# Optimization experiments

Measured on AMD Instinct MI355X. Metric: run time of the kernel, lower is better.

The kernel has to match this reference:

```python
import jax, jax.numpy as jnp
import numpy as np

HIDDEN = 2048
N_HEADS = 16
N_KV_HEADS = 4
HEAD_DIM = 128
N_REP = N_HEADS // N_KV_HEADS
BATCH = 2
SEQ = 2048
SCALE = HEAD_DIM ** -0.5
NEG = -1e9


def apply_rope(x, freqs):
    # x: (b, s, h, d); freqs: (s, d//2) angles. Interleaved-pair rotation.
    cos = jnp.cos(freqs)[None, :, None, :]
    sin = jnp.sin(freqs)[None, :, None, :]
    x1 = x[..., 0::2]
    x2 = x[..., 1::2]
    r1 = x1 * cos - x2 * sin
    r2 = x1 * sin + x2 * cos
    return jnp.stack([r1, r2], axis=-1).reshape(x.shape)


def setup_inputs() -> dict:
    key = jax.random.key(0)
    ks = jax.random.split(key, 6)
    x = jax.random.normal(ks[0], (BATCH, SEQ, HIDDEN), dtype=jnp.float32)
    wq = jax.random.normal(ks[1], (N_HEADS * HEAD_DIM, HIDDEN), dtype=jnp.float32) * 0.02
    wk = jax.random.normal(ks[2], (N_KV_HEADS * HEAD_DIM, HIDDEN), dtype=jnp.float32) * 0.02
    wv = jax.random.normal(ks[3], (N_KV_HEADS * HEAD_DIM, HIDDEN), dtype=jnp.float32) * 0.02
    wo = jax.random.normal(ks[4], (HIDDEN, N_HEADS * HEAD_DIM), dtype=jnp.float32) * 0.02
    # RoPE angle table: pos * theta^{-2i/d}
    inv_freq = 1.0 / (10000.0 ** (jnp.arange(0, HEAD_DIM, 2, dtype=jnp.float32) / HEAD_DIM))
    rope_freqs = jnp.arange(SEQ, dtype=jnp.float32)[:, None] * inv_freq[None, :]  # (S, d/2)
    # additive causal mask
    causal = jnp.tril(jnp.ones((SEQ, SEQ), dtype=bool))
    mask = jnp.where(causal, 0.0, NEG).astype(jnp.float32)[None, None]  # (1,1,S,S)
    return {"x": x, "wq": wq, "wk": wk, "wv": wv, "wo": wo,
            "rope_freqs": rope_freqs, "mask": mask}


def reference(x, wq, wk, wv, wo, rope_freqs, mask):
    b, s, _ = x.shape
    q = (x @ wq.T).reshape(b, s, N_HEADS, HEAD_DIM)
    k = (x @ wk.T).reshape(b, s, N_KV_HEADS, HEAD_DIM)
    v = (x @ wv.T).reshape(b, s, N_KV_HEADS, HEAD_DIM)
    q = apply_rope(q, rope_freqs)
    k = apply_rope(k, rope_freqs)
    new_k, new_v = k, v  # kv cache (no prior cache, start_pos=0)
    # GQA: repeat each kv head n_rep times (matches expand+reshape in source)
    k_rep = jnp.repeat(k, N_REP, axis=2)  # (b, s, n_heads, d)
    v_rep = jnp.repeat(v, N_REP, axis=2)
    scores = jnp.einsum('bqhd,bkhd->bhqk', q, k_rep) * SCALE
    scores = scores + mask
    attn = jax.nn.softmax(scores.astype(jnp.float32), axis=-1).astype(q.dtype)
    out = jnp.einsum('bhqk,bkhd->bqhd', attn, v_rep).reshape(b, s, -1)
    return out @ wo.T, (new_k, new_v)
```

## Files before the change

### kernel.cpp

```cpp
#include <hip/hip_runtime.h>
#include <hip/hip_bf16.h>

#define NH 16
#define NKV 4
#define HD 128
#define QSCALE 0.1275174272f

using bf16x8 = __attribute__((ext_vector_type(8))) __bf16;
using f32x4  = __attribute__((ext_vector_type(4))) float;
using u16x8  = __attribute__((ext_vector_type(8))) unsigned short;
using u16x2  = __attribute__((ext_vector_type(2))) unsigned short;

__device__ __forceinline__ unsigned short f2b(float f) {
  __hip_bfloat16 h = __float2bfloat16(f);
  return __builtin_bit_cast(unsigned short, h);
}
__device__ __forceinline__ float b2f(unsigned short u) {
  unsigned int v = ((unsigned int)u) << 16;
  return __builtin_bit_cast(float, v);
}

__device__ __forceinline__ void glds16(const unsigned short* g, unsigned short* l) {
  __builtin_amdgcn_global_load_lds(
      (const __attribute__((address_space(1))) unsigned int*)(const void*)g,
      (__attribute__((address_space(3))) unsigned int*)(void*)l, 16, 0, 0);
}

__global__ __launch_bounds__(256) void cvt_fused(const float* __restrict__ x,
                                                 const float* __restrict__ wq,
                                                 const float* __restrict__ wk,
                                                 const float* __restrict__ wv,
                                                 const float* __restrict__ wo,
                                                 unsigned short* __restrict__ xb,
                                                 unsigned short* __restrict__ wqkvb,
                                                 unsigned short* __restrict__ wob) {
  int i = blockIdx.x * 256 + threadIdx.x;
  const float* src;
  unsigned short* dst;
  int off;
  if (i < 1048576)      { src = x;  dst = xb;              off = i; }
  else if (i < 1572864) { src = wq; dst = wqkvb;           off = i - 1048576; }
  else if (i < 1703936) { src = wk; dst = wqkvb + 4194304; off = i - 1572864; }
  else if (i < 1835008) { src = wv; dst = wqkvb + 5242880; off = i - 1703936; }
  else                  { src = wo; dst = wob;             off = i - 1835008; }
  const float4* s4 = reinterpret_cast<const float4*>(src) + (size_t)off * 2;
  float4 v0 = s4[0], v1 = s4[1];
  u16x8 o;
  o[0] = f2b(v0.x); o[1] = f2b(v0.y); o[2] = f2b(v0.z); o[3] = f2b(v0.w);
  o[4] = f2b(v1.x); o[5] = f2b(v1.y); o[6] = f2b(v1.z); o[7] = f2b(v1.w);
  reinterpret_cast<u16x8*>(dst)[off] = o;
}

template<int CF32, int BN>
__global__ __launch_bounds__(512, 1) void gemm_full(const unsigned short* __restrict__ A,
                                                    const unsigned short* __restrict__ B,
                                                    void* __restrict__ C,
                                                    int N, int K, int nbx) {
  constexpr int BM = 128;
  constexpr int AF = 4;
  constexpr int BF = BN / 64;
  constexpr int BH = BF / 2;
  constexpr int AL = 1;
  constexpr int BL = BN / 128;
  __shared__ unsigned short As[3][BM * 32];
  __shared__ unsigned short Bs[3][BN * 32];
  const int tid = threadIdx.x, lane = tid & 63;
  const int wid = tid >> 6, wm = wid >> 2, wn = wid & 3;
  const int cpx = gridDim.x >> 3;
  const int wgid = (blockIdx.x & 7) * cpx + (blockIdx.x >> 3);
  const int bx = wgid % nbx, by = wgid / nbx;
  const int row0 = by * BM, col0 = bx * BN;
  const int fr = lane & 15, g = lane >> 4;
  const int NT = K >> 5;

  size_t offA;
  {
    int cid = tid, R = cid >> 3, phys = cid & 7, cl = phys ^ (R & 7);
    offA = (size_t)(row0 + 2 * R + (cl >> 2)) * K + (cl & 3) * 8;
  }
  size_t offB[BL];
#pragma unroll
  for (int l = 0; l < BL; l++) {
    int cid = tid + l * 512, R = cid >> 3, phys = cid & 7, cl = phys ^ (R & 7);
    offB[l] = (size_t)(col0 + 2 * R + (cl >> 2)) * K + (cl & 3) * 8;
  }

  auto stage_p0 = [&](int t, int sb) {
    int k0 = t * 32;
    glds16(A + offA + k0, &As[sb][tid * 8]);
    glds16(B + offB[0] + k0, &Bs[sb][tid * 8]);
  };
  auto stage_p1 = [&](int t, int sb) {
    int k0 = t * 32;
#pragma unroll
    for (int l = 1; l < BL; l++)
      glds16(B + offB[l] + k0, &Bs[sb][(tid + l * 512) * 8]);
  };

  auto ldfrag = [&](const unsigned short* buf, int row) {
    int R = row >> 1;
    int phys = ((((row & 1) << 2) | g) ^ (R & 7));
    return *reinterpret_cast<const bf16x8*>(&buf[R * 64 + phys * 8]);
  };

  f32x4 acc[AF][BF];
#pragma unroll
  for (int i = 0; i < AF; i++)
#pragma unroll
    for (int j = 0; j < BF; j++) acc[i][j] = f32x4{0.f, 0.f, 0.f, 0.f};

  stage_p0(0, 0); stage_p1(0, 0);
  stage_p0(1, 1); stage_p1(1, 1);
  if constexpr (AL + BL == 4) asm volatile("s_waitcnt vmcnt(4)" ::: "memory");
  else                        asm volatile("s_waitcnt vmcnt(3)" ::: "memory");
  __builtin_amdgcn_s_barrier();
  __builtin_amdgcn_sched_barrier(0);

  int rb = 0, sb = 2;
#pragma unroll 1
  for (int t = 0; t < NT; ++t) {
    const unsigned short* Ar = &As[rb][0];
    const unsigned short* Br = &Bs[rb][0];

    bf16x8 af[AF], bfr[BF];
#pragma unroll
    for (int mf = 0; mf < AF; mf++) af[mf] = ldfrag(Ar, wm * 64 + mf * 16 + fr);
#pragma unroll
    for (int nf = 0; nf < BH; nf++) bfr[nf] = ldfrag(Br, wn * (BN / 4) + nf * 16 + fr);
    if (t + 2 < NT) stage_p0(t + 2, sb);
    __builtin_amdgcn_s_barrier();
    asm volatile("s_waitcnt lgkmcnt(0)" ::: "memory");
    __builtin_amdgcn_sched_barrier(0);
    __builtin_amdgcn_s_setprio(1);
#pragma unroll
    for (int mf = 0; mf < AF; mf++)
#pragma unroll
      for (int nf = 0; nf < BH; nf++)
        acc[mf][nf] = __builtin_amdgcn_mfma_f32_16x16x32_bf16(af[mf], bfr[nf], acc[mf][nf], 0, 0, 0);
    __builtin_amdgcn_s_setprio(0);
    __builtin_amdgcn_sched_barrier(0);
    __builtin_amdgcn_s_barrier();

#pragma unroll
    for (int nf = BH; nf < BF; nf++) bfr[nf] = ldfrag(Br, wn * (BN / 4) + nf * 16 + fr);
    if (t + 2 < NT) stage_p1(t + 2, sb);
    __builtin_amdgcn_s_barrier();
    asm volatile("s_waitcnt lgkmcnt(0)" ::: "memory");
    __builtin_amdgcn_sched_barrier(0);
    __builtin_amdgcn_s_setprio(1);
#pragma unroll
    for (int mf = 0; mf < AF; mf++)
#pragma unroll
      for (int nf = BH; nf < BF; nf++)
        acc[mf][nf] = __builtin_amdgcn_mfma_f32_16x16x32_bf16(af[mf], bfr[nf], acc[mf][nf], 0, 0, 0);
    __builtin_amdgcn_s_setprio(0);
    __builtin_amdgcn_sched_barrier(0);

    if (t + 1 < NT) {
      if (t + 2 < NT) {
        if constexpr (AL + BL == 4) asm volatile("s_waitcnt vmcnt(4)" ::: "memory");
        else                        asm volatile("s_waitcnt vmcnt(3)" ::: "memory");
      } else {
        asm volatile("s_waitcnt vmcnt(0)" ::: "memory");
      }
      __builtin_amdgcn_s_barrier();
      __builtin_amdgcn_sched_barrier(0);
    }
    rb = rb == 2 ? 0 : rb + 1;
    sb = sb == 2 ? 0 : sb + 1;
  }

#pragma unroll
  for (int i = 0; i < AF; i++) {
#pragma unroll
    for (int j = 0; j < BF; j++) {
      int rbase = row0 + wm * 64 + i * 16 + g * 4;
      int cb = col0 + wn * (BN / 4) + j * 16 + fr;
#pragma unroll
      for (int r = 0; r < 4; r++) {
        if (CF32)
          reinterpret_cast<float*>(C)[(size_t)(rbase + r) * N + cb] = acc[i][j][r];
        else
          reinterpret_cast<unsigned short*>(C)[(size_t)(rbase + r) * N + cb] = f2b(acc[i][j][r]);
      }
    }
  }
}

__global__ __launch_bounds__(256) void rope_kernel(const unsigned short* __restrict__ qkv,
                                                   const float* __restrict__ freqs,
                                                   unsigned short* __restrict__ qro,
                                                   unsigned short* __restrict__ kro,
                                                   float* __restrict__ newk) {
  const int NQ = 4096 * 16 * 64;
  const int NK = 4096 * 4 * 64;
  int idx = blockIdx.x * 256 + threadIdx.x;
  if (idx >= NQ + NK) return;
  if (idx < NQ) {
    int i = idx & 63;
    int h = (idx >> 6) & 15;
    int row = idx >> 10;
    int s = row & 2047, b = row >> 11;
    float f = freqs[s * 64 + i];
    float c = cosf(f), sn = sinf(f);
    u16x2 xv = *reinterpret_cast<const u16x2*>(qkv + (size_t)row * 3072 + h * 128 + 2 * i);
    float x1 = b2f(xv.x), x2 = b2f(xv.y);
    float r1 = (x1 * c - x2 * sn) * QSCALE;
    float r2 = (x1 * sn + x2 * c) * QSCALE;
    u16x2 o; o.x = f2b(r1); o.y = f2b(r2);
    *reinterpret_cast<u16x2*>(qro + ((size_t)(b * 16 + h) * 2048 + s) * 128 + 2 * i) = o;
  } else {
    idx -= NQ;
    int i = idx & 63;
    int h = (idx >> 6) & 3;
    int row = idx >> 8;
    int s = row & 2047, b = row >> 11;
    float f = freqs[s * 64 + i];
    float c = cosf(f), sn = sinf(f);
    u16x2 xv = *reinterpret_cast<const u16x2*>(qkv + (size_t)row * 3072 + 2048 + h * 128 + 2 * i);
    float x1 = b2f(xv.x), x2 = b2f(xv.y);
    float r1 = x1 * c - x2 * sn;
    float r2 = x1 * sn + x2 * c;
    u16x2 o; o.x = f2b(r1); o.y = f2b(r2);
    *reinterpret_cast<u16x2*>(kro + ((size_t)(b * 4 + h) * 2048 + s) * 128 + 2 * i) = o;
    float2 of; of.x = r1; of.y = r2;
    *reinterpret_cast<float2*>(newk + (size_t)row * 512 + h * 128 + 2 * i) = of;
  }
}

__global__ __launch_bounds__(256) void vtrans_kernel(const unsigned short* __restrict__ qkv,
                                                     unsigned short* __restrict__ vt,
                                                     float* __restrict__ newv) {
  __shared__ unsigned short T[32][136];
  const int st = blockIdx.x;
  const int kvh = blockIdx.y & 3, b = blockIdx.y >> 2;
  const int s0 = st * 32;
  const int t = threadIdx.x;
  const int ls = t >> 3;
  const int ch = (t & 7) * 2;
  const unsigned short* src = qkv + (size_t)(b * 2048 + s0 + ls) * 3072 + 2560 + kvh * 128 + ch * 8;
  u16x8 a0 = *reinterpret_cast<const u16x8*>(src);
  u16x8 a1 = *reinterpret_cast<const u16x8*>(src + 8);
  *reinterpret_cast<u16x8*>(&T[ls][ch * 8])     = a0;
  *reinterpret_cast<u16x8*>(&T[ls][ch * 8 + 8]) = a1;
  float* nv = newv + (size_t)(b * 2048 + s0 + ls) * 512 + kvh * 128 + ch * 8;
  float4 f0, f1, f2, f3;
  f0.x = b2f(a0[0]); f0.y = b2f(a0[1]); f0.z = b2f(a0[2]); f0.w = b2f(a0[3]);
  f1.x = b2f(a0[4]); f1.y = b2f(a0[5]); f1.z = b2f(a0[6]); f1.w = b2f(a0[7]);
  f2.x = b2f(a1[0]); f2.y = b2f(a1[1]); f2.z = b2f(a1[2]); f2.w = b2f(a1[3]);
  f3.x = b2f(a1[4]); f3.y = b2f(a1[5]); f3.z = b2f(a1[6]); f3.w = b2f(a1[7]);
  reinterpret_cast<float4*>(nv)[0] = f0;
  reinterpret_cast<float4*>(nv)[1] = f1;
  reinterpret_cast<float4*>(nv)[2] = f2;
  reinterpret_cast<float4*>(nv)[3] = f3;
  __syncthreads();
  const int d = t >> 1, half = t & 1;
  unsigned short* dst = vt + ((size_t)(b * 4 + kvh) * 128 + d) * 2048 + s0 + half * 16;
  u16x8 o0, o1;
#pragma unroll
  for (int q = 0; q < 8; q++) {
    int slot = half * 16 + q;
    int kl = ((slot >> 2) & 1) * 16 + (slot >> 3) * 4 + (slot & 3);
    o0[q] = T[kl][d];
  }
#pragma unroll
  for (int q = 0; q < 8; q++) {
    int slot = half * 16 + 8 + q;
    int kl = ((slot >> 2) & 1) * 16 + (slot >> 3) * 4 + (slot & 3);
    o1[q] = T[kl][d];
  }
  reinterpret_cast<u16x8*>(dst)[0] = o0;
  reinterpret_cast<u16x8*>(dst)[1] = o1;
}

__global__ __launch_bounds__(256, 4) void attn_kernel(const unsigned short* __restrict__ qro,
                                                      const unsigned short* __restrict__ kro,
                                                      const unsigned short* __restrict__ vt,
                                                      unsigned short* __restrict__ out) {
  __shared__ unsigned short Ks[2][32 * 128];
  __shared__ unsigned short Vs[2][64 * 64];
  const int tid = threadIdx.x, lane = tid & 63, w = tid >> 6;
  const int kvhb = blockIdx.x & 7;
  const int kvh = kvhb & 3, b = kvhb >> 2;
  const int t = 127 - (blockIdx.x >> 3);
  const int h = kvh * 4 + w;
  const int qbase = t * 16;
  const int fr = lane & 15, g = lane >> 4, fk = g * 8;
  const unsigned short* Kp = kro + (size_t)(b * 4 + kvh) * 2048 * 128;
  const unsigned short* Vtp = vt + (size_t)(b * 4 + kvh) * 128 * 2048;
  const unsigned short* Qp = qro + ((size_t)(b * 16 + h) * 2048 + qbase) * 128;

  bf16x8 qf[4];
#pragma unroll
  for (int kk = 0; kk < 4; kk++)
    qf[kk] = *reinterpret_cast<const bf16x8*>(Qp + fr * 128 + kk * 32 + fk);

  u16x8 onesu;
#pragma unroll
  for (int j = 0; j < 8; j++) onesu[j] = 0x3F80;
  bf16x8 ones = __builtin_bit_cast(bf16x8, onesu);

  f32x4 o[8];
#pragma unroll
  for (int dt = 0; dt < 8; dt++) o[dt] = f32x4{0.f, 0.f, 0.f, 0.f};
  f32x4 dacc = f32x4{0.f, 0.f, 0.f, 0.f};
  const int qrow_s = qbase + fr;
  const int nfull = (qbase >= 31) ? ((qbase - 31) >> 5) + 1 : 0;
  const int niter = nfull + 1;

  const int krow = w * 8 + (lane >> 4);
  const int kcol = lane & 15;
  const int vrow = w * 16 + (lane >> 3);
  const int vcol = lane & 7;

  auto stage = [&](int kv0, int buf) {
    unsigned short* Kb = &Ks[buf][0];
    unsigned short* Vb = &Vs[buf][0];
#pragma unroll
    for (int j = 0; j < 2; j++) {
      int r = krow + j * 4;
      glds16(Kp + (size_t)(kv0 + r) * 128 + ((kcol ^ (r & 7)) * 8),
             Kb + (w * 8 + j * 4) * 128);
    }
#pragma unroll
    for (int j = 0; j < 2; j++) {
      int r = vrow + j * 8;
      int u = vcol ^ (r & 7);
      int d = 2 * r + (u >> 2);
      glds16(Vtp + (size_t)d * 2048 + kv0 + (u & 3) * 8,
             Vb + (w * 16 + j * 8) * 64);
    }
  };

  auto step = [&](int kv0, bool mask, int buf) {
    const unsigned short* Kb = &Ks[buf][0];
    const unsigned short* Vb = &Vs[buf][0];
    f32x4 sc[2];
    sc[0] = sc[1] = f32x4{0.f, 0.f, 0.f, 0.f};
    __builtin_amdgcn_s_setprio(1);
#pragma unroll
    for (int kk = 0; kk < 4; kk++) {
      int blk = ((kk * 4 + g) ^ (fr & 7)) * 8;
      bf16x8 ka0 = *reinterpret_cast<const bf16x8*>(Kb + (fr +  0) * 128 + blk);
      bf16x8 ka1 = *reinterpret_cast<const bf16x8*>(Kb + (fr + 16) * 128 + blk);
      sc[0] = __builtin_amdgcn_mfma_f32_16x16x32_bf16(ka0, qf[kk], sc[0], 0, 0, 0);
      sc[1] = __builtin_amdgcn_mfma_f32_16x16x32_bf16(ka1, qf[kk], sc[1], 0, 0, 0);
    }
    __builtin_amdgcn_s_setprio(0);
#pragma unroll
    for (int s = 0; s < 2; s++)
#pragma unroll
      for (int r = 0; r < 4; r++) {
        float v = sc[s][r];
        if (mask && (kv0 + 16 * s + 4 * g + r > qrow_s)) v = -1e30f;
        sc[s][r] = __builtin_amdgcn_exp2f(v);
      }
    u16x8 pau;
#pragma unroll
    for (int j = 0; j < 4; j++) {
      pau[j]     = f2b(sc[0][j]);
      pau[4 + j] = f2b(sc[1][j]);
    }
    bf16x8 pa = __builtin_bit_cast(bf16x8, pau);
    dacc = __builtin_amdgcn_mfma_f32_16x16x32_bf16(pa, ones, dacc, 0, 0, 0);
    __builtin_amdgcn_s_setprio(1);
#pragma unroll
    for (int dt = 0; dt < 8; dt++) {
      int jr = dt * 8 + (fr >> 1);
      int c = ((fr & 1) * 4 + g) ^ (fr >> 1);
      bf16x8 vf = *reinterpret_cast<const bf16x8*>(Vb + jr * 64 + c * 8);
      o[dt] = __builtin_amdgcn_mfma_f32_16x16x32_bf16(pa, vf, o[dt], 0, 0, 0);
    }
    __builtin_amdgcn_s_setprio(0);
  };

  stage(0, 0);
  int buf = 0;
  for (int i = 0; i < niter; i++) {
    __syncthreads();
    if (i + 1 < niter) stage((i + 1) * 32, buf ^ 1);
    step(i * 32, i == nfull, buf);
    buf ^= 1;
  }

#pragma unroll
  for (int r = 0; r < 4; r++) {
    float inv = 1.0f / dacc[r];
    int qrow = qbase + g * 4 + r;
    size_t rowoff = ((size_t)b * 2048 + qrow) * 2048 + (size_t)h * 128;
#pragma unroll
    for (int dt = 0; dt < 8; dt++)
      out[rowoff + dt * 16 + fr] = f2b(o[dt][r] * inv);
  }
}

extern "C" void kernel_launch(void* const* d_in, const int* in_sizes, int n_in,
                              void* d_out, int out_size, void* d_ws, size_t ws_size,
                              hipStream_t stream) {
  const float* x  = (const float*)d_in[0];
  const float* wq = (const float*)d_in[1];
  const float* wk = (const float*)d_in[2];
  const float* wv = (const float*)d_in[3];
  const float* wo = (const float*)d_in[4];
  const float* freqs = (const float*)d_in[5];

  char* ws = (char*)d_ws;
  unsigned short* xb    = (unsigned short*)(ws);
  unsigned short* attn  = xb;
  unsigned short* wqkvb = (unsigned short*)(ws + 16777216);
  unsigned short* wob   = (unsigned short*)(ws + 29360128);
  unsigned short* qkv   = (unsigned short*)(ws + 37748736);
  unsigned short* qro   = (unsigned short*)(ws + 62914560);
  unsigned short* kro   = (unsigned short*)(ws + 79691776);
  unsigned short* vt    = (unsigned short*)(ws + 83886080);

  float* out_o = (float*)d_out;
  float* out_k = (float*)d_out + 8388608;
  float* out_v = (float*)d_out + 10485760;

  cvt_fused<<<9216, 256, 0, stream>>>(x, wq, wk, wv, wo, xb, wqkvb, wob);

  gemm_full<0, 384><<<256, 512, 0, stream>>>(xb, wqkvb, qkv, 3072, 2048, 8);

  rope_kernel<<<20480, 256, 0, stream>>>(qkv, freqs, qro, kro, out_k);
  vtrans_kernel<<<dim3(64, 8), 256, 0, stream>>>(qkv, vt, out_v);

  attn_kernel<<<1024, 256, 0, stream>>>(qro, kro, vt, attn);

  gemm_full<1, 256><<<256, 512, 0, stream>>>(attn, wob, out_o, 2048, 2048, 8);
}
```

Measured before the change: 206.2 us.

## Process 32 query rows per warp in attention to reuse K/V tiles

Each warp now handles two 16-row query sub-tiles instead of one, so every K and V fragment loaded from shared memory feeds twice as many MFMAs. The grid is halved to 512 blocks and launch bounds drop to 2 blocks per SM to make room for the doubled accumulators. This targets LDS/global traffic per FLOP in the attention kernel. In exchange it uses more registers, gives lower occupancy, adds some wasted masked work on the diagonal tile, and leaves fewer blocks to balance the causal workload.

```diff
diff --git a/kernel.cpp b/kernel.cpp
--- a/kernel.cpp
+++ b/kernel.cpp
@@ -273,7 +273,7 @@
   reinterpret_cast<u16x8*>(dst)[1] = o1;
 }
 
-__global__ __launch_bounds__(256, 4) void attn_kernel(const unsigned short* __restrict__ qro,
+__global__ __launch_bounds__(256, 2) void attn_kernel(const unsigned short* __restrict__ qro,
                                                       const unsigned short* __restrict__ kro,
                                                       const unsigned short* __restrict__ vt,
                                                       unsigned short* __restrict__ out) {
@@ -282,31 +282,33 @@
   const int tid = threadIdx.x, lane = tid & 63, w = tid >> 6;
   const int kvhb = blockIdx.x & 7;
   const int kvh = kvhb & 3, b = kvhb >> 2;
-  const int t = 127 - (blockIdx.x >> 3);
+  const int t = 63 - (blockIdx.x >> 3);
   const int h = kvh * 4 + w;
-  const int qbase = t * 16;
+  const int qbase = t * 32;
   const int fr = lane & 15, g = lane >> 4, fk = g * 8;
   const unsigned short* Kp = kro + (size_t)(b * 4 + kvh) * 2048 * 128;
   const unsigned short* Vtp = vt + (size_t)(b * 4 + kvh) * 128 * 2048;
   const unsigned short* Qp = qro + ((size_t)(b * 16 + h) * 2048 + qbase) * 128;
 
-  bf16x8 qf[4];
-#pragma unroll
-  for (int kk = 0; kk < 4; kk++)
-    qf[kk] = *reinterpret_cast<const bf16x8*>(Qp + fr * 128 + kk * 32 + fk);
+  bf16x8 qf0[4], qf1[4];
+#pragma unroll
+  for (int kk = 0; kk < 4; kk++) {
+    qf0[kk] = *reinterpret_cast<const bf16x8*>(Qp + fr * 128 + kk * 32 + fk);
+    qf1[kk] = *reinterpret_cast<const bf16x8*>(Qp + (16 + fr) * 128 + kk * 32 + fk);
+  }
 
   u16x8 onesu;
 #pragma unroll
   for (int j = 0; j < 8; j++) onesu[j] = 0x3F80;
   bf16x8 ones = __builtin_bit_cast(bf16x8, onesu);
 
-  f32x4 o[8];
-#pragma unroll
-  for (int dt = 0; dt < 8; dt++) o[dt] = f32x4{0.f, 0.f, 0.f, 0.f};
-  f32x4 dacc = f32x4{0.f, 0.f, 0.f, 0.f};
-  const int qrow_s = qbase + fr;
-  const int nfull = (qbase >= 31) ? ((qbase - 31) >> 5) + 1 : 0;
-  const int niter = nfull + 1;
+  f32x4 o0[8], o1[8];
+#pragma unroll
+  for (int dt = 0; dt < 8; dt++) { o0[dt] = f32x4{0.f, 0.f, 0.f, 0.f}; o1[dt] = f32x4{0.f, 0.f, 0.f, 0.f}; }
+  f32x4 dacc0 = f32x4{0.f, 0.f, 0.f, 0.f};
+  f32x4 dacc1 = f32x4{0.f, 0.f, 0.f, 0.f};
+  const int qrow0 = qbase + fr, qrow1 = qbase + 16 + fr;
+  const int niter = t + 1;
 
   const int krow = w * 8 + (lane >> 4);
   const int kcol = lane & 15;
@@ -335,41 +337,53 @@
   auto step = [&](int kv0, bool mask, int buf) {
     const unsigned short* Kb = &Ks[buf][0];
     const unsigned short* Vb = &Vs[buf][0];
-    f32x4 sc[2];
-    sc[0] = sc[1] = f32x4{0.f, 0.f, 0.f, 0.f};
+    f32x4 sA[2], sB[2];
+    sA[0] = sA[1] = f32x4{0.f, 0.f, 0.f, 0.f};
+    sB[0] = sB[1] = f32x4{0.f, 0.f, 0.f, 0.f};
     __builtin_amdgcn_s_setprio(1);
 #pragma unroll
     for (int kk = 0; kk < 4; kk++) {
       int blk = ((kk * 4 + g) ^ (fr & 7)) * 8;
       bf16x8 ka0 = *reinterpret_cast<const bf16x8*>(Kb + (fr +  0) * 128 + blk);
       bf16x8 ka1 = *reinterpret_cast<const bf16x8*>(Kb + (fr + 16) * 128 + blk);
-      sc[0] = __builtin_amdgcn_mfma_f32_16x16x32_bf16(ka0, qf[kk], sc[0], 0, 0, 0);
-      sc[1] = __builtin_amdgcn_mfma_f32_16x16x32_bf16(ka1, qf[kk], sc[1], 0, 0, 0);
+      sA[0] = __builtin_amdgcn_mfma_f32_16x16x32_bf16(ka0, qf0[kk], sA[0], 0, 0, 0);
+      sB[0] = __builtin_amdgcn_mfma_f32_16x16x32_bf16(ka0, qf1[kk], sB[0], 0, 0, 0);
+      sA[1] = __builtin_amdgcn_mfma_f32_16x16x32_bf16(ka1, qf0[kk], sA[1], 0, 0, 0);
+      sB[1] = __builtin_amdgcn_mfma_f32_16x16x32_bf16(ka1, qf1[kk], sB[1], 0, 0, 0);
     }
     __builtin_amdgcn_s_setprio(0);
 #pragma unroll
-    for (int s = 0; s < 2; s++)
+    for (int hh = 0; hh < 2; hh++)
 #pragma unroll
       for (int r = 0; r < 4; r++) {
-        float v = sc[s][r];
-        if (mask && (kv0 + 16 * s + 4 * g + r > qrow_s)) v = -1e30f;
-        sc[s][r] = __builtin_amdgcn_exp2f(v);
+        int kvidx = kv0 + 16 * hh + 4 * g + r;
+        float vA = sA[hh][r];
+        float vB = sB[hh][r];
+        if (mask && (kvidx > qrow0)) vA = -1e30f;
+        if (mask && (kvidx > qrow1)) vB = -1e30f;
+        sA[hh][r] = __builtin_amdgcn_exp2f(vA);
+        sB[hh][r] = __builtin_amdgcn_exp2f(vB);
       }
-    u16x8 pau;
+    u16x8 pau, pbu;
 #pragma unroll
     for (int j = 0; j < 4; j++) {
-      pau[j]     = f2b(sc[0][j]);
-      pau[4 + j] = f2b(sc[1][j]);
+      pau[j]     = f2b(sA[0][j]);
+      pau[4 + j] = f2b(sA[1][j]);
+      pbu[j]     = f2b(sB[0][j]);
+      pbu[4 + j] = f2b(sB[1][j]);
     }
     bf16x8 pa = __builtin_bit_cast(bf16x8, pau);
-    dacc = __builtin_amdgcn_mfma_f32_16x16x32_bf16(pa, ones, dacc, 0, 0, 0);
+    bf16x8 pb = __builtin_bit_cast(bf16x8, pbu);
+    dacc0 = __builtin_amdgcn_mfma_f32_16x16x32_bf16(pa, ones, dacc0, 0, 0, 0);
+    dacc1 = __builtin_amdgcn_mfma_f32_16x16x32_bf16(pb, ones, dacc1, 0, 0, 0);
     __builtin_amdgcn_s_setprio(1);
 #pragma unroll
     for (int dt = 0; dt < 8; dt++) {
       int jr = dt * 8 + (fr >> 1);
       int c = ((fr & 1) * 4 + g) ^ (fr >> 1);
       bf16x8 vf = *reinterpret_cast<const bf16x8*>(Vb + jr * 64 + c * 8);
-      o[dt] = __builtin_amdgcn_mfma_f32_16x16x32_bf16(pa, vf, o[dt], 0, 0, 0);
+      o0[dt] = __builtin_amdgcn_mfma_f32_16x16x32_bf16(pa, vf, o0[dt], 0, 0, 0);
+      o1[dt] = __builtin_amdgcn_mfma_f32_16x16x32_bf16(pb, vf, o1[dt], 0, 0, 0);
     }
     __builtin_amdgcn_s_setprio(0);
   };
@@ -379,18 +393,23 @@
   for (int i = 0; i < niter; i++) {
     __syncthreads();
     if (i + 1 < niter) stage((i + 1) * 32, buf ^ 1);
-    step(i * 32, i == nfull, buf);
+    step(i * 32, i == niter - 1, buf);
     buf ^= 1;
   }
 
 #pragma unroll
   for (int r = 0; r < 4; r++) {
-    float inv = 1.0f / dacc[r];
-    int qrow = qbase + g * 4 + r;
-    size_t rowoff = ((size_t)b * 2048 + qrow) * 2048 + (size_t)h * 128;
-#pragma unroll
-    for (int dt = 0; dt < 8; dt++)
-      out[rowoff + dt * 16 + fr] = f2b(o[dt][r] * inv);
+    float inv0 = 1.0f / dacc0[r];
+    float inv1 = 1.0f / dacc1[r];
+    int q0 = qbase + g * 4 + r;
+    int q1 = qbase + 16 + g * 4 + r;
+    size_t ro0 = ((size_t)b * 2048 + q0) * 2048 + (size_t)h * 128;
+    size_t ro1 = ((size_t)b * 2048 + q1) * 2048 + (size_t)h * 128;
+#pragma unroll
+    for (int dt = 0; dt < 8; dt++) {
+      out[ro0 + dt * 16 + fr] = f2b(o0[dt][r] * inv0);
+      out[ro1 + dt * 16 + fr] = f2b(o1[dt][r] * inv1);
+    }
   }
 }
 
@@ -425,7 +444,7 @@
   rope_kernel<<<20480, 256, 0, stream>>>(qkv, freqs, qro, kro, out_k);
   vtrans_kernel<<<dim3(64, 8), 256, 0, stream>>>(qkv, vt, out_v);
 
-  attn_kernel<<<1024, 256, 0, stream>>>(qro, kro, vt, attn);
+  attn_kernel<<<512, 256, 0, stream>>>(qro, kro, vt, attn);
 
   gemm_full<1, 256><<<256, 512, 0, stream>>>(attn, wob, out_o, 2048, 2048, 8);
 }
```

New measurement: 214.1 us. 1.04x slower.

## Fuse RoPE, V transpose and KV cache writes into QKV GEMM epilogue

Applied to the files above, without the earlier changes.

The standalone rope and V-transpose kernels are removed. The QKV GEMM epilogue now applies RoPE using lane shuffles for the interleaved pairs, writes the rotated Q and K plus the fp32 new_k, and stores the transposed bf16 V along with the fp32 new_v. A cos/sin table is precomputed inside the conversion kernel. This removes the bf16 qkv intermediate round-trip and two kernel launches, at the cost of scattered 2-byte epilogue stores and extra table loads in the GEMM.

```diff
diff --git a/kernel.cpp b/kernel.cpp
--- a/kernel.cpp
+++ b/kernel.cpp
@@ -9,6 +9,7 @@
 using bf16x8 = __attribute__((ext_vector_type(8))) __bf16;
 using f32x4  = __attribute__((ext_vector_type(4))) float;
 using u16x8  = __attribute__((ext_vector_type(8))) unsigned short;
+using u16x4  = __attribute__((ext_vector_type(4))) unsigned short;
 using u16x2  = __attribute__((ext_vector_type(2))) unsigned short;
 
 __device__ __forceinline__ unsigned short f2b(float f) {
@@ -31,10 +32,19 @@
                                                  const float* __restrict__ wk,
                                                  const float* __restrict__ wv,
                                                  const float* __restrict__ wo,
+                                                 const float* __restrict__ freqs,
                                                  unsigned short* __restrict__ xb,
                                                  unsigned short* __restrict__ wqkvb,
-                                                 unsigned short* __restrict__ wob) {
+                                                 unsigned short* __restrict__ wob,
+                                                 float2* __restrict__ cs_tab) {
   int i = blockIdx.x * 256 + threadIdx.x;
+  if (i >= 2359296) {
+    int k = i - 2359296;
+    float f = freqs[k];
+    float2 cs; cs.x = cosf(f); cs.y = sinf(f);
+    cs_tab[k] = cs;
+    return;
+  }
   const float* src;
   unsigned short* dst;
   int off;
@@ -49,6 +59,172 @@
   o[0] = f2b(v0.x); o[1] = f2b(v0.y); o[2] = f2b(v0.z); o[3] = f2b(v0.w);
   o[4] = f2b(v1.x); o[5] = f2b(v1.y); o[6] = f2b(v1.z); o[7] = f2b(v1.w);
   reinterpret_cast<u16x8*>(dst)[off] = o;
+}
+
+__global__ __launch_bounds__(512, 1) void gemm_qkv(const unsigned short* __restrict__ A,
+                                                   const unsigned short* __restrict__ B,
+                                                   const float2* __restrict__ cs_tab,
+                                                   unsigned short* __restrict__ qro,
+                                                   unsigned short* __restrict__ kro,
+                                                   unsigned short* __restrict__ vt,
+                                                   float* __restrict__ newk,
+                                                   float* __restrict__ newv,
+                                                   int K) {
+  constexpr int BN = 384;
+  constexpr int AF = 4, BF = 6, BH = 3, BL = 3;
+  __shared__ unsigned short As[3][128 * 32];
+  __shared__ unsigned short Bs[3][BN * 32];
+  const int tid = threadIdx.x, lane = tid & 63;
+  const int wid = tid >> 6, wm = wid >> 2, wn = wid & 3;
+  const int cpx = gridDim.x >> 3;
+  const int wgid = (blockIdx.x & 7) * cpx + (blockIdx.x >> 3);
+  const int bx = wgid % 8, by = wgid / 8;
+  const int row0 = by * 128, col0 = bx * BN;
+  const int fr = lane & 15, g = lane >> 4;
+  const int NT = K >> 5;
+
+  size_t offA;
+  {
+    int cid = tid, R = cid >> 3, phys = cid & 7, cl = phys ^ (R & 7);
+    offA = (size_t)(row0 + 2 * R + (cl >> 2)) * K + (cl & 3) * 8;
+  }
+  size_t offB[BL];
+#pragma unroll
+  for (int l = 0; l < BL; l++) {
+    int cid = tid + l * 512, R = cid >> 3, phys = cid & 7, cl = phys ^ (R & 7);
+    offB[l] = (size_t)(col0 + 2 * R + (cl >> 2)) * K + (cl & 3) * 8;
+  }
+
+  auto stage_p0 = [&](int t, int sb) {
+    int k0 = t * 32;
+    glds16(A + offA + k0, &As[sb][tid * 8]);
+    glds16(B + offB[0] + k0, &Bs[sb][tid * 8]);
+  };
+  auto stage_p1 = [&](int t, int sb) {
+    int k0 = t * 32;
+#pragma unroll
+    for (int l = 1; l < BL; l++)
+      glds16(B + offB[l] + k0, &Bs[sb][(tid + l * 512) * 8]);
+  };
+
+  auto ldfrag = [&](const unsigned short* buf, int row) {
+    int R = row >> 1;
+    int phys = ((((row & 1) << 2) | g) ^ (R & 7));
+    return *reinterpret_cast<const bf16x8*>(&buf[R * 64 + phys * 8]);
+  };
+
+  f32x4 acc[AF][BF];
+#pragma unroll
+  for (int i = 0; i < AF; i++)
+#pragma unroll
+    for (int j = 0; j < BF; j++) acc[i][j] = f32x4{0.f, 0.f, 0.f, 0.f};
+
+  stage_p0(0, 0); stage_p1(0, 0);
+  stage_p0(1, 1); stage_p1(1, 1);
+  asm volatile("s_waitcnt vmcnt(4)" ::: "memory");
+  __builtin_amdgcn_s_barrier();
+  __builtin_amdgcn_sched_barrier(0);
+
+  int rb = 0, sb = 2;
+#pragma unroll 1
+  for (int t = 0; t < NT; ++t) {
+    const unsigned short* Ar = &As[rb][0];
+    const unsigned short* Br = &Bs[rb][0];
+
+    bf16x8 af[AF], bfr[BF];
+#pragma unroll
+    for (int mf = 0; mf < AF; mf++) af[mf] = ldfrag(Ar, wm * 64 + mf * 16 + fr);
+#pragma unroll
+    for (int nf = 0; nf < BH; nf++) bfr[nf] = ldfrag(Br, wn * 96 + nf * 16 + fr);
+    if (t + 2 < NT) stage_p0(t + 2, sb);
+    __builtin_amdgcn_s_barrier();
+    asm volatile("s_waitcnt lgkmcnt(0)" ::: "memory");
+    __builtin_amdgcn_sched_barrier(0);
+    __builtin_amdgcn_s_setprio(1);
+#pragma unroll
+    for (int mf = 0; mf < AF; mf++)
+#pragma unroll
+      for (int nf = 0; nf < BH; nf++)
+        acc[mf][nf] = __builtin_amdgcn_mfma_f32_16x16x32_bf16(af[mf], bfr[nf], acc[mf][nf], 0, 0, 0);
+    __builtin_amdgcn_s_setprio(0);
+    __builtin_amdgcn_sched_barrier(0);
+    __builtin_amdgcn_s_barrier();
+
+#pragma unroll
+    for (int nf = BH; nf < BF; nf++) bfr[nf] = ldfrag(Br, wn * 96 + nf * 16 + fr);
+    if (t + 2 < NT) stage_p1(t + 2, sb);
+    __builtin_amdgcn_s_barrier();
+    asm volatile("s_waitcnt lgkmcnt(0)" ::: "memory");
+    __builtin_amdgcn_sched_barrier(0);
+    __builtin_amdgcn_s_setprio(1);
+#pragma unroll
+    for (int mf = 0; mf < AF; mf++)
+#pragma unroll
+      for (int nf = BH; nf < BF; nf++)
+        acc[mf][nf] = __builtin_amdgcn_mfma_f32_16x16x32_bf16(af[mf], bfr[nf], acc[mf][nf], 0, 0, 0);
+    __builtin_amdgcn_s_setprio(0);
+    __builtin_amdgcn_sched_barrier(0);
+
+    if (t + 1 < NT) {
+      if (t + 2 < NT) asm volatile("s_waitcnt vmcnt(4)" ::: "memory");
+      else            asm volatile("s_waitcnt vmcnt(0)" ::: "memory");
+      __builtin_amdgcn_s_barrier();
+      __builtin_amdgcn_sched_barrier(0);
+    }
+    rb = rb == 2 ? 0 : rb + 1;
+    sb = sb == 2 ? 0 : sb + 1;
+  }
+
+#pragma unroll
+  for (int i = 0; i < AF; i++) {
+    int rbase = row0 + wm * 64 + i * 16 + g * 4;
+    int bb = rbase >> 11;
+    int sr0 = rbase & 2047;
+#pragma unroll
+    for (int j = 0; j < BF; j++) {
+      int cb = col0 + wn * 96 + j * 16 + fr;
+      int d = cb & 127;
+      if (cb < 2048) {
+        int hq = cb >> 7;
+        unsigned short* qp = qro + ((size_t)(bb * 16 + hq) * 2048 + sr0) * 128 + d;
+#pragma unroll
+        for (int r = 0; r < 4; r++) {
+          float own = acc[i][j][r];
+          float par = __shfl_xor(own, 1);
+          float2 cs = cs_tab[(sr0 + r) * 64 + (d >> 1)];
+          float o = (fr & 1) ? (par * cs.y + own * cs.x) : (own * cs.x - par * cs.y);
+          qp[(size_t)r * 128] = f2b(o * QSCALE);
+        }
+      } else if (cb < 2560) {
+        int kvh = (cb >> 7) & 3;
+        unsigned short* kp = kro + ((size_t)(bb * 4 + kvh) * 2048 + sr0) * 128 + d;
+        float* nk = newk + ((size_t)bb * 2048 + sr0) * 512 + kvh * 128 + d;
+#pragma unroll
+        for (int r = 0; r < 4; r++) {
+          float own = acc[i][j][r];
+          float par = __shfl_xor(own, 1);
+          float2 cs = cs_tab[(sr0 + r) * 64 + (d >> 1)];
+          float o = (fr & 1) ? (par * cs.y + own * cs.x) : (own * cs.x - par * cs.y);
+          kp[(size_t)r * 128] = f2b(o);
+          nk[(size_t)r * 512] = o;
+        }
+      } else {
+        int kvh = (cb >> 7) & 3;
+        float* nv = newv + ((size_t)bb * 2048 + sr0) * 512 + kvh * 128 + d;
+        u16x4 pack;
+#pragma unroll
+        for (int r = 0; r < 4; r++) {
+          float v = acc[i][j][r];
+          nv[(size_t)r * 512] = v;
+          pack[r] = f2b(v);
+        }
+        int kl = sr0 & 31;
+        int slotb = ((kl >> 2) & 3) * 8 + (kl >> 4) * 4;
+        *reinterpret_cast<u16x4*>(vt + ((size_t)(bb * 4 + kvh) * 128 + d) * 2048
+                                  + (sr0 & ~31) + slotb) = pack;
+      }
+    }
+  }
 }
 
 template<int CF32, int BN>
@@ -187,92 +363,6 @@
   }
 }
 
-__global__ __launch_bounds__(256) void rope_kernel(const unsigned short* __restrict__ qkv,
-                                                   const float* __restrict__ freqs,
-                                                   unsigned short* __restrict__ qro,
-                                                   unsigned short* __restrict__ kro,
-                                                   float* __restrict__ newk) {
-  const int NQ = 4096 * 16 * 64;
-  const int NK = 4096 * 4 * 64;
-  int idx = blockIdx.x * 256 + threadIdx.x;
-  if (idx >= NQ + NK) return;
-  if (idx < NQ) {
-    int i = idx & 63;
-    int h = (idx >> 6) & 15;
-    int row = idx >> 10;
-    int s = row & 2047, b = row >> 11;
-    float f = freqs[s * 64 + i];
-    float c = cosf(f), sn = sinf(f);
-    u16x2 xv = *reinterpret_cast<const u16x2*>(qkv + (size_t)row * 3072 + h * 128 + 2 * i);
-    float x1 = b2f(xv.x), x2 = b2f(xv.y);
-    float r1 = (x1 * c - x2 * sn) * QSCALE;
-    float r2 = (x1 * sn + x2 * c) * QSCALE;
-    u16x2 o; o.x = f2b(r1); o.y = f2b(r2);
-    *reinterpret_cast<u16x2*>(qro + ((size_t)(b * 16 + h) * 2048 + s) * 128 + 2 * i) = o;
-  } else {
-    idx -= NQ;
-    int i = idx & 63;
-    int h = (idx >> 6) & 3;
-    int row = idx >> 8;
-    int s = row & 2047, b = row >> 11;
-    float f = freqs[s * 64 + i];
-    float c = cosf(f), sn = sinf(f);
-    u16x2 xv = *reinterpret_cast<const u16x2*>(qkv + (size_t)row * 3072 + 2048 + h * 128 + 2 * i);
-    float x1 = b2f(xv.x), x2 = b2f(xv.y);
-    float r1 = x1 * c - x2 * sn;
-    float r2 = x1 * sn + x2 * c;
-    u16x2 o; o.x = f2b(r1); o.y = f2b(r2);
-    *reinterpret_cast<u16x2*>(kro + ((size_t)(b * 4 + h) * 2048 + s) * 128 + 2 * i) = o;
-    float2 of; of.x = r1; of.y = r2;
-    *reinterpret_cast<float2*>(newk + (size_t)row * 512 + h * 128 + 2 * i) = of;
-  }
-}
-
-__global__ __launch_bounds__(256) void vtrans_kernel(const unsigned short* __restrict__ qkv,
-                                                     unsigned short* __restrict__ vt,
-                                                     float* __restrict__ newv) {
-  __shared__ unsigned short T[32][136];
-  const int st = blockIdx.x;
-  const int kvh = blockIdx.y & 3, b = blockIdx.y >> 2;
-  const int s0 = st * 32;
-  const int t = threadIdx.x;
-  const int ls = t >> 3;
-  const int ch = (t & 7) * 2;
-  const unsigned short* src = qkv + (size_t)(b * 2048 + s0 + ls) * 3072 + 2560 + kvh * 128 + ch * 8;
-  u16x8 a0 = *reinterpret_cast<const u16x8*>(src);
-  u16x8 a1 = *reinterpret_cast<const u16x8*>(src + 8);
-  *reinterpret_cast<u16x8*>(&T[ls][ch * 8])     = a0;
-  *reinterpret_cast<u16x8*>(&T[ls][ch * 8 + 8]) = a1;
-  float* nv = newv + (size_t)(b * 2048 + s0 + ls) * 512 + kvh * 128 + ch * 8;
-  float4 f0, f1, f2, f3;
-  f0.x = b2f(a0[0]); f0.y = b2f(a0[1]); f0.z = b2f(a0[2]); f0.w = b2f(a0[3]);
-  f1.x = b2f(a0[4]); f1.y = b2f(a0[5]); f1.z = b2f(a0[6]); f1.w = b2f(a0[7]);
-  f2.x = b2f(a1[0]); f2.y = b2f(a1[1]); f2.z = b2f(a1[2]); f2.w = b2f(a1[3]);
-  f3.x = b2f(a1[4]); f3.y = b2f(a1[5]); f3.z = b2f(a1[6]); f3.w = b2f(a1[7]);
-  reinterpret_cast<float4*>(nv)[0] = f0;
-  reinterpret_cast<float4*>(nv)[1] = f1;
-  reinterpret_cast<float4*>(nv)[2] = f2;
-  reinterpret_cast<float4*>(nv)[3] = f3;
-  __syncthreads();
-  const int d = t >> 1, half = t & 1;
-  unsigned short* dst = vt + ((size_t)(b * 4 + kvh) * 128 + d) * 2048 + s0 + half * 16;
-  u16x8 o0, o1;
-#pragma unroll
-  for (int q = 0; q < 8; q++) {
-    int slot = half * 16 + q;
-    int kl = ((slot >> 2) & 1) * 16 + (slot >> 3) * 4 + (slot & 3);
-    o0[q] = T[kl][d];
-  }
-#pragma unroll
-  for (int q = 0; q < 8; q++) {
-    int slot = half * 16 + 8 + q;
-    int kl = ((slot >> 2) & 1) * 16 + (slot >> 3) * 4 + (slot & 3);
-    o1[q] = T[kl][d];
-  }
-  reinterpret_cast<u16x8*>(dst)[0] = o0;
-  reinterpret_cast<u16x8*>(dst)[1] = o1;
-}
-
 __global__ __launch_bounds__(256, 4) void attn_kernel(const unsigned short* __restrict__ qro,
                                                       const unsigned short* __restrict__ kro,
                                                       const unsigned short* __restrict__ vt,
@@ -409,7 +499,7 @@
   unsigned short* attn  = xb;
   unsigned short* wqkvb = (unsigned short*)(ws + 16777216);
   unsigned short* wob   = (unsigned short*)(ws + 29360128);
-  unsigned short* qkv   = (unsigned short*)(ws + 37748736);
+  float2*         cstab = (float2*)(ws + 37748736);
   unsigned short* qro   = (unsigned short*)(ws + 62914560);
   unsigned short* kro   = (unsigned short*)(ws + 79691776);
   unsigned short* vt    = (unsigned short*)(ws + 83886080);
@@ -418,12 +508,9 @@
   float* out_k = (float*)d_out + 8388608;
   float* out_v = (float*)d_out + 10485760;
 
-  cvt_fused<<<9216, 256, 0, stream>>>(x, wq, wk, wv, wo, xb, wqkvb, wob);
-
-  gemm_full<0, 384><<<256, 512, 0, stream>>>(xb, wqkvb, qkv, 3072, 2048, 8);
-
-  rope_kernel<<<20480, 256, 0, stream>>>(qkv, freqs, qro, kro, out_k);
-  vtrans_kernel<<<dim3(64, 8), 256, 0, stream>>>(qkv, vt, out_v);
+  cvt_fused<<<9728, 256, 0, stream>>>(x, wq, wk, wv, wo, freqs, xb, wqkvb, wob, cstab);
+
+  gemm_qkv<<<256, 512, 0, stream>>>(xb, wqkvb, cstab, qro, kro, vt, out_k, out_v, 2048);
 
   attn_kernel<<<1024, 256, 0, stream>>>(qro, kro, vt, attn);
 
```

Measured after the change: 195.3 us. -5.3%, faster.
